# Performance work log

Hardware: AMD Instinct MI355X
Metric: run time of the kernel (lower is better)

Reference implementation:

```python
import jax, jax.numpy as jnp
import numpy as np

H = 32  # hidden_size
I = 1   # input_size
O = 1   # output_size


def setup_inputs() -> dict:
    key = jax.random.key(0)
    ks = jax.random.split(key, 7)
    T, B = 2048, 2048
    s_ih = 1.0 / np.sqrt(H)
    return {
        "x": jax.random.normal(ks[0], (T, B, I), dtype=jnp.float32),
        "W_ih": jax.random.uniform(ks[1], (4 * H, I), jnp.float32, -s_ih, s_ih),
        "W_hh": jax.random.uniform(ks[2], (4 * H, H), jnp.float32, -s_ih, s_ih),
        "b_ih": jax.random.uniform(ks[3], (4 * H,), jnp.float32, -s_ih, s_ih),
        "b_hh": jax.random.uniform(ks[4], (4 * H,), jnp.float32, -s_ih, s_ih),
        "W_out": jax.random.uniform(ks[5], (O, H), jnp.float32, -s_ih, s_ih),
        "b_out": jax.random.uniform(ks[6], (O,), jnp.float32, -s_ih, s_ih),
    }


def _lstm(x, W_ih, W_hh, b_ih, b_hh):
    T, B, _ = x.shape
    # Precompute input contribution for all timesteps: [T, B, 4H]
    x_gates = jnp.einsum('tbi,gi->tbg', x, W_ih) + b_ih + b_hh

    def step(carry, xg):
        h, c = carry
        gates = xg + h @ W_hh.T  # [B, 4H]
        i, f, g, o = jnp.split(gates, 4, axis=-1)  # PyTorch gate order i,f,g,o
        i = jax.nn.sigmoid(i)
        f = jax.nn.sigmoid(f)
        g = jnp.tanh(g)
        o = jax.nn.sigmoid(o)
        c = f * c + i * g
        h = o * jnp.tanh(c)
        return (h, c), h

    h0 = jnp.zeros((B, H), dtype=x.dtype)
    c0 = jnp.zeros((B, H), dtype=x.dtype)
    (hT, cT), r_out = jax.lax.scan(step, (h0, c0), x_gates)
    return r_out, (hT[None], cT[None])  # match PyTorch [num_layers, B, H] state


def reference(x, W_ih, W_hh, b_ih, b_hh, W_out, b_out):
    r_out, state = _lstm(x, W_ih, W_hh, b_ih, b_hh)  # [T, B, H]
    outs = jnp.einsum('tbh,oh->tbo', r_out, W_out) + b_out  # [T, B, O]
    return outs, state
```

## Files before the change

kernel.cpp:

```cpp
#include <hip/hip_runtime.h>


namespace {
constexpr int T_ = 2048;
constexpr int B_ = 2048;
constexpr int H_ = 32;
constexpr int EPB = 4;
constexpr int CHUNK = 64;
constexpr int NCH = T_ / CHUNK;
constexpr int OUTS = T_ * B_;
constexpr float L2E = 1.442695040888963f;

typedef float v2f __attribute__((ext_vector_type(2)));
typedef float v4f __attribute__((ext_vector_type(4)));

__device__ __forceinline__ float rcp_(float v){ return __builtin_amdgcn_rcpf(v); }
__device__ __forceinline__ float ex2_(float v){ return __builtin_amdgcn_exp2f(v); }

template <int CTRL, int RM, int BM, bool BC>
__device__ __forceinline__ float dpp_movf(float src) {
    return __builtin_bit_cast(float,
        __builtin_amdgcn_update_dpp(0, __builtin_bit_cast(int, src),
                                    CTRL, RM, BM, BC));
}
template <int CTRL, int RM, int BM, bool BC>
__device__ __forceinline__ float dpp_add(float acc, float src) {
    return acc + dpp_movf<CTRL,RM,BM,BC>(src);
}
}

__global__ __launch_bounds__(256, 2) void lstm_fused8(
    const float* __restrict__ x,
    const float* __restrict__ W_ih,
    const float* __restrict__ W_hh,
    const float* __restrict__ b_ih,
    const float* __restrict__ b_hh,
    const float* __restrict__ W_out,
    const float* __restrict__ b_out,
    float* __restrict__ out)
{
    const int l  = threadIdx.x & 63;
    const int wv = threadIdx.x >> 6;
    const int j  = l >> 1;
    const int kh = l & 1;
    const int e  = blockIdx.x * EPB + wv;
    const bool odd = (kh != 0);

    __shared__ __align__(16) float hbuf[EPB][H_];

    const float sI = -L2E, sF = -L2E, sG = 2.0f*L2E, sO = -L2E;

    v2f wI[8], wF[8], wG[8], wO[8];
#pragma unroll
    for (int q = 0; q < 8; ++q) {
        const int k = kh*16 + 2*q;
        wI[q] = (v2f){ W_hh[(0*H_+j)*H_+k]*sI, W_hh[(0*H_+j)*H_+k+1]*sI };
        wF[q] = (v2f){ W_hh[(1*H_+j)*H_+k]*sF, W_hh[(1*H_+j)*H_+k+1]*sF };
        wG[q] = (v2f){ W_hh[(2*H_+j)*H_+k]*sG, W_hh[(2*H_+j)*H_+k+1]*sG };
        wO[q] = (v2f){ W_hh[(3*H_+j)*H_+k]*sO, W_hh[(3*H_+j)*H_+k+1]*sO };
    }

    const float wxI = W_ih[0*H_+j]*sI, wxF = W_ih[1*H_+j]*sF;
    const float wxG = W_ih[2*H_+j]*sG, wxO = W_ih[3*H_+j]*sO;
    const float bI = (b_ih[0*H_+j]+b_hh[0*H_+j])*sI;
    const float bF = (b_ih[1*H_+j]+b_hh[1*H_+j])*sF;
    const float bG = (b_ih[2*H_+j]+b_hh[2*H_+j])*sG;
    const float bO = (b_ih[3*H_+j]+b_hh[3*H_+j])*sO;
    const float cP0 = odd ? 1.0f : 0.0f;
    const float cP1 = odd ? -2.0f : 1.0f;
    const float woutM = odd ? 0.0f : W_out[j];
    const float bout  = b_out[0];

    float c = 0.0f, h = 0.0f;
    hbuf[wv][j] = 0.0f;
    __asm__ __volatile__("" ::: "memory");
    const float* hp = &hbuf[wv][kh*16];
    v4f h4[4];
#pragma unroll
    for (int q = 0; q < 4; ++q) h4[q] = ((const v4f*)hp)[q];

    float xcur = x[l * B_ + e];
    int outOff = e;

    for (int ch = 0; ch < NCH; ++ch) {
#pragma unroll
        for (int q = 0; q < 8; ++q) {
            __asm__ __volatile__("" : "+v"(wI[q]), "+v"(wF[q]));
            __asm__ __volatile__("" : "+v"(wG[q]), "+v"(wO[q]));
        }
        float xnext = 0.0f;
        if (ch + 1 < NCH) xnext = x[((ch+1)*CHUNK + l) * B_ + e];
#pragma unroll 8
        for (int s = 0; s < CHUNK; ++s) {
            const float xk = __builtin_bit_cast(float,
                __builtin_amdgcn_readlane(__builtin_bit_cast(int, xcur), s));
            const float xtI = bI + xk*wxI;
            const float xtF = bF + xk*wxF;
            const float xtG = bG + xk*wxG;
            const float xtO = bO + xk*wxO;
            v2f aI2, aF2, aG2, aO2;
            {
                const v2f p0 = (v2f){h4[0].x, h4[0].y};
                aI2 = wI[0]*p0; aF2 = wF[0]*p0; aG2 = wG[0]*p0; aO2 = wO[0]*p0;
            }
#pragma unroll
            for (int q = 1; q < 8; ++q) {
                const v4f hv = h4[q>>1];
                const v2f pp = (q&1) ? (v2f){hv.z, hv.w} : (v2f){hv.x, hv.y};
                aI2 += wI[q]*pp; aF2 += wF[q]*pp;
                aG2 += wG[q]*pp; aO2 += wO[q]*pp;
            }
            float aI = aI2.x + aI2.y, aF = aF2.x + aF2.y;
            float aG = aG2.x + aG2.y, aO = aO2.x + aO2.y;
            aI = dpp_add<0xB1,0xF,0xF,true>(aI, aI);
            aF = dpp_add<0xB1,0xF,0xF,true>(aF, aF);
            aG = dpp_add<0xB1,0xF,0xF,true>(aG, aG);
            aO = dpp_add<0xB1,0xF,0xF,true>(aO, aO);
            aI += xtI; aF += xtF; aG += xtG; aO += xtO;
            const float aP = odd ? aG : aI;
            const float aQ = odd ? aO : aF;
            const float actP = cP0 + cP1 * rcp_(1.0f + ex2_(aP));
            const float actQ = rcp_(1.0f + ex2_(aQ));
            const float nbP = dpp_movf<0xB1,0xF,0xF,true>(actP);
            const float nbQ = dpp_movf<0xB1,0xF,0xF,true>(actQ);
            const float iv = odd ? nbP : actP;
            const float fv = odd ? nbQ : actQ;
            const float gv = odd ? actP : nbP;
            const float ov = odd ? actQ : nbQ;
            c = fv*c + iv*gv;
            const float tc = 1.0f - 2.0f*rcp_(1.0f + ex2_((2.0f*L2E)*c));
            h = ov*tc;
            hbuf[wv][j] = h;
            __asm__ __volatile__("" ::: "memory");
#pragma unroll
            for (int q = 0; q < 4; ++q) h4[q] = ((const v4f*)hp)[q];
            float pr = h * woutM;
            pr = dpp_add<0x111,0xF,0xF,true>(pr, pr);
            pr = dpp_add<0x112,0xF,0xF,true>(pr, pr);
            pr = dpp_add<0x114,0xF,0xF,true>(pr, pr);
            pr = dpp_add<0x118,0xF,0xF,true>(pr, pr);
            pr = dpp_add<0x142,0xA,0xF,false>(pr, pr);
            const float s0 = __builtin_bit_cast(float,
                __builtin_amdgcn_readlane(__builtin_bit_cast(int, pr), 31));
            const float s1 = __builtin_bit_cast(float,
                __builtin_amdgcn_readlane(__builtin_bit_cast(int, pr), 63));
            if (l == 0) out[outOff] = s0 + s1 + bout;
            outOff += B_;
        }
        xcur = xnext;
    }
    if (!odd) {
        out[OUTS + e*H_ + j] = h;
        out[OUTS + B_*H_ + e*H_ + j] = c;
    }
}

extern "C" void kernel_launch(void* const* d_in, const int* in_sizes, int n_in,
                              void* d_out, int out_size, void* d_ws, size_t ws_size,
                              hipStream_t stream) {
    const float* x     = (const float*)d_in[0];
    const float* W_ih  = (const float*)d_in[1];
    const float* W_hh  = (const float*)d_in[2];
    const float* b_ih  = (const float*)d_in[3];
    const float* b_hh  = (const float*)d_in[4];
    const float* W_out = (const float*)d_in[5];
    const float* b_out = (const float*)d_in[6];
    lstm_fused8<<<dim3(B_ / EPB), dim3(EPB * 64), 0, stream>>>(
        x, W_ih, W_hh, b_ih, b_hh, W_out, b_out, (float*)d_out);
}
```

Measured before the change: 835.3 us.

## Split work by gate pairs per lane instead of K halves, drop DPP reductions

Each lane pair now splits the work by gate instead of by hidden-input half. One lane computes the full 32-wide dot products for gates i and f, the other for g and o, so the per-gate cross-lane DPP add is no longer needed. The cell state is kept pre-scaled by 2*log2(e), which removes a multiply from the tanh path, and the output reduction uses a full-wave DPP sum instead of two readlanes. Each lane still does the same number of FMAs, now on twice the K length with two interleaved accumulators. The trade-off is that the whole 32-element h vector is read from LDS on every step.

```diff
diff --git a/kernel.cpp b/kernel.cpp
--- a/kernel.cpp
+++ b/kernel.cpp
@@ -5,7 +5,7 @@
 constexpr int T_ = 2048;
 constexpr int B_ = 2048;
 constexpr int H_ = 32;
-constexpr int EPB = 4;
+constexpr int WPB = 4;
 constexpr int CHUNK = 64;
 constexpr int NCH = T_ / CHUNK;
 constexpr int OUTS = T_ * B_;
@@ -27,9 +27,18 @@
 __device__ __forceinline__ float dpp_add(float acc, float src) {
     return acc + dpp_movf<CTRL,RM,BM,BC>(src);
 }
+__device__ __forceinline__ float wave_sum64(float v) {
+    v = dpp_add<0x111,0xF,0xF,true >(v, v);
+    v = dpp_add<0x112,0xF,0xF,true >(v, v);
+    v = dpp_add<0x114,0xF,0xF,true >(v, v);
+    v = dpp_add<0x118,0xF,0xF,true >(v, v);
+    v = dpp_add<0x142,0xA,0xF,false>(v, v);
+    v = dpp_add<0x143,0x8,0xF,false>(v, v);
+    return v;
+}
 }
 
-__global__ __launch_bounds__(256, 2) void lstm_fused8(
+__global__ __launch_bounds__(256, 2) void lstm_fused12(
     const float* __restrict__ x,
     const float* __restrict__ W_ih,
     const float* __restrict__ W_hh,
@@ -42,116 +51,94 @@
     const int l  = threadIdx.x & 63;
     const int wv = threadIdx.x >> 6;
     const int j  = l >> 1;
-    const int kh = l & 1;
-    const int e  = blockIdx.x * EPB + wv;
-    const bool odd = (kh != 0);
+    const int gp = l & 1;
+    const int e  = blockIdx.x * WPB + wv;
+    const bool odd = (gp != 0);
 
-    __shared__ __align__(16) float hbuf[EPB][H_];
+    __shared__ __align__(16) float hbuf[WPB][H_];
 
-    const float sI = -L2E, sF = -L2E, sG = 2.0f*L2E, sO = -L2E;
+    const int gA = gp * 2;
+    const int gB = gp * 2 + 1;
+    const float sA = odd ? 2.0f*L2E : -L2E;
+    const float sB = -L2E;
+    const float cA0 = odd ? 2.0f*L2E : 0.0f;
+    const float cA1 = odd ? -4.0f*L2E : 1.0f;
 
-    v2f wI[8], wF[8], wG[8], wO[8];
+    v2f wA[H_/2], wB[H_/2];
 #pragma unroll
-    for (int q = 0; q < 8; ++q) {
-        const int k = kh*16 + 2*q;
-        wI[q] = (v2f){ W_hh[(0*H_+j)*H_+k]*sI, W_hh[(0*H_+j)*H_+k+1]*sI };
-        wF[q] = (v2f){ W_hh[(1*H_+j)*H_+k]*sF, W_hh[(1*H_+j)*H_+k+1]*sF };
-        wG[q] = (v2f){ W_hh[(2*H_+j)*H_+k]*sG, W_hh[(2*H_+j)*H_+k+1]*sG };
-        wO[q] = (v2f){ W_hh[(3*H_+j)*H_+k]*sO, W_hh[(3*H_+j)*H_+k+1]*sO };
+    for (int k2 = 0; k2 < H_/2; ++k2) {
+        const float* rA = W_hh + (gA*H_ + j) * H_;
+        const float* rB = W_hh + (gB*H_ + j) * H_;
+        wA[k2] = (v2f){ rA[2*k2] * sA, rA[2*k2+1] * sA };
+        wB[k2] = (v2f){ rB[2*k2] * sB, rB[2*k2+1] * sB };
+    }
+#pragma unroll
+    for (int k2 = 0; k2 < H_/2; ++k2) {
+        __asm__ __volatile__("" : "+v"(wA[k2]), "+v"(wB[k2]));
     }
 
-    const float wxI = W_ih[0*H_+j]*sI, wxF = W_ih[1*H_+j]*sF;
-    const float wxG = W_ih[2*H_+j]*sG, wxO = W_ih[3*H_+j]*sO;
-    const float bI = (b_ih[0*H_+j]+b_hh[0*H_+j])*sI;
-    const float bF = (b_ih[1*H_+j]+b_hh[1*H_+j])*sF;
-    const float bG = (b_ih[2*H_+j]+b_hh[2*H_+j])*sG;
-    const float bO = (b_ih[3*H_+j]+b_hh[3*H_+j])*sO;
-    const float cP0 = odd ? 1.0f : 0.0f;
-    const float cP1 = odd ? -2.0f : 1.0f;
+    const float wxA = W_ih[gA*H_+j] * sA;
+    const float wxB = W_ih[gB*H_+j] * sB;
+    const float bA  = (b_ih[gA*H_+j] + b_hh[gA*H_+j]) * sA;
+    const float bB  = (b_ih[gB*H_+j] + b_hh[gB*H_+j]) * sB;
     const float woutM = odd ? 0.0f : W_out[j];
     const float bout  = b_out[0];
 
-    float c = 0.0f, h = 0.0f;
+    float c2 = 0.0f, h = 0.0f;
     hbuf[wv][j] = 0.0f;
     __asm__ __volatile__("" ::: "memory");
-    const float* hp = &hbuf[wv][kh*16];
-    v4f h4[4];
+    v4f hq[H_/4];
 #pragma unroll
-    for (int q = 0; q < 4; ++q) h4[q] = ((const v4f*)hp)[q];
+    for (int q = 0; q < H_/4; ++q)
+        hq[q] = ((const v4f*)&hbuf[wv][0])[q];
 
     float xcur = x[l * B_ + e];
     int outOff = e;
 
     for (int ch = 0; ch < NCH; ++ch) {
-#pragma unroll
-        for (int q = 0; q < 8; ++q) {
-            __asm__ __volatile__("" : "+v"(wI[q]), "+v"(wF[q]));
-            __asm__ __volatile__("" : "+v"(wG[q]), "+v"(wO[q]));
-        }
         float xnext = 0.0f;
         if (ch + 1 < NCH) xnext = x[((ch+1)*CHUNK + l) * B_ + e];
 #pragma unroll 8
         for (int s = 0; s < CHUNK; ++s) {
             const float xk = __builtin_bit_cast(float,
                 __builtin_amdgcn_readlane(__builtin_bit_cast(int, xcur), s));
-            const float xtI = bI + xk*wxI;
-            const float xtF = bF + xk*wxF;
-            const float xtG = bG + xk*wxG;
-            const float xtO = bO + xk*wxO;
-            v2f aI2, aF2, aG2, aO2;
-            {
-                const v2f p0 = (v2f){h4[0].x, h4[0].y};
-                aI2 = wI[0]*p0; aF2 = wF[0]*p0; aG2 = wG[0]*p0; aO2 = wO[0]*p0;
+            v2f aA0 = {bA + xk*wxA, 0.f}, aA1 = {0.f, 0.f};
+            v2f aB0 = {bB + xk*wxB, 0.f}, aB1 = {0.f, 0.f};
+#pragma unroll
+            for (int q = 0; q < H_/4; ++q) {
+                const v2f hlo = (v2f){ hq[q].x, hq[q].y };
+                const v2f hhi = (v2f){ hq[q].z, hq[q].w };
+                aA0 += wA[2*q] * hlo;  aA1 += wA[2*q+1] * hhi;
+                aB0 += wB[2*q] * hlo;  aB1 += wB[2*q+1] * hhi;
             }
-#pragma unroll
-            for (int q = 1; q < 8; ++q) {
-                const v4f hv = h4[q>>1];
-                const v2f pp = (q&1) ? (v2f){hv.z, hv.w} : (v2f){hv.x, hv.y};
-                aI2 += wI[q]*pp; aF2 += wF[q]*pp;
-                aG2 += wG[q]*pp; aO2 += wO[q]*pp;
-            }
-            float aI = aI2.x + aI2.y, aF = aF2.x + aF2.y;
-            float aG = aG2.x + aG2.y, aO = aO2.x + aO2.y;
-            aI = dpp_add<0xB1,0xF,0xF,true>(aI, aI);
-            aF = dpp_add<0xB1,0xF,0xF,true>(aF, aF);
-            aG = dpp_add<0xB1,0xF,0xF,true>(aG, aG);
-            aO = dpp_add<0xB1,0xF,0xF,true>(aO, aO);
-            aI += xtI; aF += xtF; aG += xtG; aO += xtO;
-            const float aP = odd ? aG : aI;
-            const float aQ = odd ? aO : aF;
-            const float actP = cP0 + cP1 * rcp_(1.0f + ex2_(aP));
-            const float actQ = rcp_(1.0f + ex2_(aQ));
-            const float nbP = dpp_movf<0xB1,0xF,0xF,true>(actP);
-            const float nbQ = dpp_movf<0xB1,0xF,0xF,true>(actQ);
-            const float iv = odd ? nbP : actP;
-            const float fv = odd ? nbQ : actQ;
-            const float gv = odd ? actP : nbP;
-            const float ov = odd ? actQ : nbQ;
-            c = fv*c + iv*gv;
-            const float tc = 1.0f - 2.0f*rcp_(1.0f + ex2_((2.0f*L2E)*c));
-            h = ov*tc;
+            const v2f aAv = aA0 + aA1, aBv = aB0 + aB1;
+            const float aA = aAv.x + aAv.y;
+            const float aB = aBv.x + aBv.y;
+            const float actA = cA0 + cA1 * rcp_(1.0f + ex2_(aA));
+            const float actB = rcp_(1.0f + ex2_(aB));
+            const float nA = dpp_movf<0xB1,0xF,0xF,true>(actA);
+            const float nB = dpp_movf<0xB1,0xF,0xF,true>(actB);
+            const float iv  = odd ? nA : actA;
+            const float fv  = odd ? nB : actB;
+            const float gv2 = odd ? actA : nA;
+            const float ov  = odd ? actB : nB;
+            c2 = fv * c2 + iv * gv2;
+            const float tc = 1.0f - 2.0f * rcp_(1.0f + ex2_(c2));
+            h = ov * tc;
             hbuf[wv][j] = h;
             __asm__ __volatile__("" ::: "memory");
 #pragma unroll
-            for (int q = 0; q < 4; ++q) h4[q] = ((const v4f*)hp)[q];
-            float pr = h * woutM;
-            pr = dpp_add<0x111,0xF,0xF,true>(pr, pr);
-            pr = dpp_add<0x112,0xF,0xF,true>(pr, pr);
-            pr = dpp_add<0x114,0xF,0xF,true>(pr, pr);
-            pr = dpp_add<0x118,0xF,0xF,true>(pr, pr);
-            pr = dpp_add<0x142,0xA,0xF,false>(pr, pr);
-            const float s0 = __builtin_bit_cast(float,
-                __builtin_amdgcn_readlane(__builtin_bit_cast(int, pr), 31));
-            const float s1 = __builtin_bit_cast(float,
-                __builtin_amdgcn_readlane(__builtin_bit_cast(int, pr), 63));
-            if (l == 0) out[outOff] = s0 + s1 + bout;
+            for (int q = 0; q < H_/4; ++q)
+                hq[q] = ((const v4f*)&hbuf[wv][0])[q];
+            const float pr = wave_sum64(h * woutM);
+            if (l == 63) out[outOff] = pr + bout;
             outOff += B_;
         }
         xcur = xnext;
     }
     if (!odd) {
         out[OUTS + e*H_ + j] = h;
-        out[OUTS + B_*H_ + e*H_ + j] = c;
+        out[OUTS + B_*H_ + e*H_ + j] = c2 * (0.5f / L2E);
     }
 }
 
@@ -165,6 +152,6 @@
     const float* b_hh  = (const float*)d_in[4];
     const float* W_out = (const float*)d_in[5];
     const float* b_out = (const float*)d_in[6];
-    lstm_fused8<<<dim3(B_ / EPB), dim3(EPB * 64), 0, stream>>>(
+    lstm_fused12<<<dim3(B_ / WPB), dim3(WPB * 64), 0, stream>>>(
         x, W_ih, W_hh, b_ih, b_hh, W_out, b_out, (float*)d_out);
 }
```

Result: faster. 767.4 us (-8.1%).
